# Kernel tuning notes

Measured on AMD Instinct MI355X. Metric: run time of the kernel, lower is better.

## Reference

```python
import jax, jax.numpy as jnp
import numpy as np

N_NODE = 50000
N_EDGE = 640000
IN_DIM = 128
OUT_DIM = 128
ATTN_DIM = 128
N_REL = 500
REL_VOCAB = 2 * N_REL + 3  # 1003


def setup_inputs() -> dict:
    key = jax.random.key(0)
    ks = jax.random.split(key, 10)
    hidden = jax.random.normal(ks[0], (N_NODE, IN_DIM), dtype=jnp.float32)
    sub = jax.random.randint(ks[1], (N_EDGE,), 0, N_NODE)
    rel = jax.random.randint(ks[2], (N_EDGE,), 0, REL_VOCAB)
    obj = jax.random.randint(ks[3], (N_EDGE,), 0, N_NODE)
    zero = jnp.zeros((N_EDGE,), dtype=jnp.int64 if jax.config.read('jax_enable_x64') else jnp.int32)
    # edges layout: [:,2]=rel, [:,4]=sub, [:,5]=obj (other columns unused)
    edges = jnp.stack([zero, zero, rel, zero, sub, obj], axis=1)
    old_nodes_new_idx = jax.random.randint(ks[4], (N_NODE,), 0, N_NODE)
    s = 1.0 / np.sqrt(IN_DIM)
    rela_embed = jax.random.normal(ks[5], (REL_VOCAB, IN_DIM), dtype=jnp.float32)
    Ws_attn = jax.random.uniform(ks[6], (IN_DIM, ATTN_DIM), minval=-s, maxval=s, dtype=jnp.float32)
    Wr_attn = jax.random.uniform(ks[7], (IN_DIM, ATTN_DIM), minval=-s, maxval=s, dtype=jnp.float32)
    sa = 1.0 / np.sqrt(ATTN_DIM)
    w_alpha_w = jax.random.uniform(ks[8], (ATTN_DIM, 1), minval=-sa, maxval=sa, dtype=jnp.float32)
    w_alpha_b = jnp.zeros((1,), dtype=jnp.float32)
    W_h = jax.random.uniform(ks[9], (IN_DIM, OUT_DIM), minval=-s, maxval=s, dtype=jnp.float32)
    return {
        'hidden': hidden, 'edges': edges, 'n_node': N_NODE,
        'old_nodes_new_idx': old_nodes_new_idx,
        'rela_embed': rela_embed, 'Ws_attn': Ws_attn, 'Wr_attn': Wr_attn,
        'w_alpha_w': w_alpha_w, 'w_alpha_b': w_alpha_b, 'W_h': W_h,
    }


def reference(hidden, edges, n_node, old_nodes_new_idx,
              rela_embed, Ws_attn, Wr_attn, w_alpha_w, w_alpha_b, W_h):
    sub = edges[:, 4]
    rel = edges[:, 2]
    obj = edges[:, 5]
    hs = hidden[sub]                 # [E, in_dim] gather
    hr = rela_embed[rel]             # [E, in_dim] gather
    message = hs + hr                # [E, in_dim]
    attn_h = jax.nn.relu(hs @ Ws_attn + hr @ Wr_attn)          # [E, attn_dim]
    alpha = jax.nn.sigmoid(attn_h @ w_alpha_w + w_alpha_b)     # [E, 1]
    message = alpha * message
    message_agg = jax.ops.segment_sum(message, obj, num_segments=n_node)  # [N, in_dim]
    hidden_new = message_agg @ W_h   # act is identity by default
    return hidden_new
```

## Files before the change

### kernel.cpp

```cpp
#include <hip/hip_runtime.h>

typedef float f4 __attribute__((ext_vector_type(4)));
typedef float f2 __attribute__((ext_vector_type(2)));
typedef float f32x4 __attribute__((ext_vector_type(4)));
typedef short bf16x8 __attribute__((ext_vector_type(8)));
typedef unsigned short u16x8 __attribute__((ext_vector_type(8)));

__device__ inline unsigned short f2bf(float f) {
  unsigned u = __float_as_uint(f);
  return (unsigned short)((u + 0x7FFF + ((u >> 16) & 1)) >> 16);
}

__global__ __launch_bounds__(256) void prep(
    const float* __restrict__ Ws, const float* __restrict__ Wr,
    const float* __restrict__ Wh, const int* __restrict__ edges, int n_edge,
    unsigned short* __restrict__ WsT, unsigned short* __restrict__ WrT,
    unsigned short* __restrict__ WhT, int* __restrict__ counts,
    uint2* __restrict__ epk) {
  const int t = threadIdx.x;
  int b = blockIdx.x;
  if (b < 192) {
    int wsel = b >> 6;
    const float* W = wsel == 0 ? Ws : (wsel == 1 ? Wr : Wh);
    unsigned short* WT = wsel == 0 ? WsT : (wsel == 1 ? WrT : WhT);
    int e = (b & 63) * 256 + t;
    int cc = e >> 7, kk = e & 127;
    WT[e] = f2bf(W[kk * 128 + cc]);
    return;
  }
  b -= 192;
  int e = b * 256 + t;
  if (e < n_edge) {
    int rel = edges[(size_t)e * 6 + 2];
    int2 so = *(const int2*)(edges + (size_t)e * 6 + 4);
    atomicAdd(&counts[so.y], 1);
    epk[e] = make_uint2((unsigned)so.x | ((unsigned)rel << 17), (unsigned)so.y);
  }
}

__global__ __launch_bounds__(256) void gemm_dual(
    const float* __restrict__ hidden, int M, int nbN,
    const float* __restrict__ rela, int relv,
    const unsigned short* __restrict__ WsT, const unsigned short* __restrict__ WrT,
    const unsigned short* __restrict__ WhT,
    char* __restrict__ rec, char* __restrict__ relrec) {
  __shared__ __align__(16) char lds[81920];
  const int t = threadIdx.x;
  int b = blockIdx.x;
  const float* src;
  const unsigned short* WxT;
  char* out;
  int rows, row0;
  if (b < nbN) { src = hidden; WxT = WsT; out = rec; rows = M; row0 = b * 64; }
  else { src = rela; WxT = WrT; out = relrec; rows = relv; row0 = (b - nbN) * 64; }

#pragma unroll
  for (int i = 0; i < 8; ++i) {
    int m = i * 256 + t;
    int sw = (m * 16) ^ (((m >> 4) & 7) << 4);
    *(u16x8*)(lds + 16384 + sw) = ((const u16x8*)WxT)[m];
    *(u16x8*)(lds + 49152 + sw) = ((const u16x8*)WhT)[m];
  }
#pragma unroll
  for (int i = 0; i < 4; ++i) {
    int m = i * 256 + t;
    int r = m >> 4, c = m & 15;
    int gr = row0 + r;
    if (gr > rows - 1) gr = rows - 1;
    const float* s = src + (size_t)gr * 128 + c * 8;
    f4 lo = *(const f4*)s, hi = *(const f4*)(s + 4);
    u16x8 v;
    v[0] = f2bf(lo.x); v[1] = f2bf(lo.y); v[2] = f2bf(lo.z); v[3] = f2bf(lo.w);
    v[4] = f2bf(hi.x); v[5] = f2bf(hi.y); v[6] = f2bf(hi.z); v[7] = f2bf(hi.w);
    *(u16x8*)(lds + ((m * 16) ^ ((r & 7) << 4))) = v;
  }
  __syncthreads();

  const int w = t >> 6, l = t & 63, lr = l & 15, lg = l >> 4;
  const int rowA = w * 16 + lr;
  bf16x8 afr[4];
#pragma unroll
  for (int k0 = 0; k0 < 4; ++k0)
    afr[k0] = *(const bf16x8*)(lds + rowA * 256 + ((k0 * 64 + lg * 16) ^ ((rowA & 7) << 4)));

  {
    f32x4 acc[8] = {};
#pragma unroll
    for (int k0 = 0; k0 < 4; ++k0) {
      int kb = k0 * 64 + lg * 16;
#pragma unroll
      for (int c0 = 0; c0 < 8; ++c0) {
        int cr = c0 * 16 + lr;
        bf16x8 bfr = *(const bf16x8*)(lds + 16384 + cr * 256 + (kb ^ ((cr & 7) << 4)));
        acc[c0] = __builtin_amdgcn_mfma_f32_16x16x32_bf16(afr[k0], bfr, acc[c0], 0, 0, 0);
      }
    }
#pragma unroll
    for (int c0 = 0; c0 < 8; ++c0) {
      int col = c0 * 16 + lr;
#pragma unroll
      for (int j = 0; j < 4; ++j) {
        int grow = row0 + w * 16 + lg * 4 + j;
        if (grow < rows) {
          unsigned pk = __builtin_amdgcn_cvt_pk_fp8_f32(acc[c0][j], acc[c0][j], 0, false);
          *(unsigned char*)(out + (size_t)grow * 384 + 256 + col) = (unsigned char)pk;
        }
      }
    }
  }
  {
    f32x4 acc[8] = {};
#pragma unroll
    for (int k0 = 0; k0 < 4; ++k0) {
      int kb = k0 * 64 + lg * 16;
#pragma unroll
      for (int c0 = 0; c0 < 8; ++c0) {
        int cr = c0 * 16 + lr;
        bf16x8 bfr = *(const bf16x8*)(lds + 49152 + cr * 256 + (kb ^ ((cr & 7) << 4)));
        acc[c0] = __builtin_amdgcn_mfma_f32_16x16x32_bf16(afr[k0], bfr, acc[c0], 0, 0, 0);
      }
    }
#pragma unroll
    for (int c0 = 0; c0 < 8; ++c0) {
      int col = c0 * 16 + lr;
#pragma unroll
      for (int j = 0; j < 4; ++j) {
        int grow = row0 + w * 16 + lg * 4 + j;
        if (grow < rows)
          *(unsigned short*)(out + (size_t)grow * 384 + col * 2) = f2bf(acc[c0][j]);
      }
    }
  }
}

__global__ __launch_bounds__(256) void scan_lookback(
    const int* __restrict__ counts, int M, int n_edge, int* __restrict__ status,
    int* __restrict__ offsets, int* __restrict__ cursor) {
  const int t = threadIdx.x, b = blockIdx.x;
  const int idx = b * 256 + t;
  int c = (idx < M) ? counts[idx] : 0;
  const int lane = t & 63, w = t >> 6;
  int s = c;
  for (int off = 1; off < 64; off <<= 1) {
    int o = __shfl_up(s, off, 64);
    if (lane >= off) s += o;
  }
  __shared__ int wsum[4], wpre[4];
  __shared__ int blk_prefix;
  if (lane == 63) wsum[w] = s;
  __syncthreads();
  if (t == 0) {
    int r = 0;
#pragma unroll
    for (int i = 0; i < 4; ++i) { wpre[i] = r; r += wsum[i]; }
    unsigned pub = ((b == 0 ? 2u : 1u) << 30) | (unsigned)r;
    __hip_atomic_store(&status[b], (int)pub, __ATOMIC_RELEASE, __HIP_MEMORY_SCOPE_AGENT);
    if (b == 0) blk_prefix = 0;
  }
  __syncthreads();
  if (b > 0 && w == 0) {
    int prefix = 0;
    int k = b - 1;
    for (;;) {
      int j = k - lane;
      unsigned v;
      if (j >= 0) {
        do {
          v = (unsigned)__hip_atomic_load(&status[j], __ATOMIC_ACQUIRE,
                                          __HIP_MEMORY_SCOPE_AGENT);
        } while ((v >> 30) == 0u);
      } else {
        v = 2u << 30;
      }
      int val = (int)(v & 0x3FFFFFFFu);
      unsigned long long incl = __ballot((v >> 30) == 2u);
      int l = (int)__ffsll(incl) - 1;
      int contrib = (l >= 0) ? ((lane <= l) ? val : 0) : val;
#pragma unroll
      for (int off = 32; off; off >>= 1) contrib += __shfl_xor(contrib, off, 64);
      prefix += contrib;
      if (l >= 0) break;
      k -= 64;
    }
    if (lane == 0) {
      blk_prefix = prefix;
      int total = wpre[3] + wsum[3];
      __hip_atomic_store(&status[b], (int)((2u << 30) | (unsigned)(prefix + total)),
                         __ATOMIC_RELEASE, __HIP_MEMORY_SCOPE_AGENT);
    }
  }
  __syncthreads();
  int excl = blk_prefix + wpre[w] + s - c;
  if (idx < M) { offsets[idx] = excl; cursor[idx] = excl; }
  if (idx == 0) offsets[M] = n_edge;
}

__global__ __launch_bounds__(256) void scatter_kernel(const uint2* __restrict__ epk,
                                                      int n_edge, int* __restrict__ cursor,
                                                      unsigned* __restrict__ esr) {
  int e = blockIdx.x * 256 + threadIdx.x;
  if (e < n_edge) {
    uint2 pe = epk[e];
    int pos = atomicAdd(&cursor[pe.y], 1);
    esr[pos] = pe.x;
  }
}

template <bool HI>
__device__ inline f2 pk8(unsigned u) {
  return __builtin_amdgcn_cvt_pk_f32_fp8(u, HI);
}

__device__ inline float edge_alpha(uint2 as, uint2 ar, const f2* wap, float bb) {
  f2 s0 = pk8<false>(as.x) + pk8<false>(ar.x);
  f2 s1 = pk8<true>(as.x) + pk8<true>(ar.x);
  f2 s2 = pk8<false>(as.y) + pk8<false>(ar.y);
  f2 s3 = pk8<true>(as.y) + pk8<true>(ar.y);
  s0.x = fmaxf(s0.x, 0.f); s0.y = fmaxf(s0.y, 0.f);
  s1.x = fmaxf(s1.x, 0.f); s1.y = fmaxf(s1.y, 0.f);
  s2.x = fmaxf(s2.x, 0.f); s2.y = fmaxf(s2.y, 0.f);
  s3.x = fmaxf(s3.x, 0.f); s3.y = fmaxf(s3.y, 0.f);
  f2 pp = s0 * wap[0];
  pp += s1 * wap[1];
  pp += s2 * wap[2];
  pp += s3 * wap[3];
  float p = pp.x + pp.y;
#pragma unroll
  for (int off = 1; off <= 8; off <<= 1) p += __shfl_xor(p, off, 64);
  return __builtin_amdgcn_rcpf(1.f + __builtin_amdgcn_exp2f(-(p + bb)));
}

__global__ __launch_bounds__(256) void node_agg(
    const int* __restrict__ offsets, const unsigned* __restrict__ esr,
    const char* __restrict__ rec, const char* __restrict__ relrec,
    float* __restrict__ out,
    const float* __restrict__ w_alpha, const float* __restrict__ w_b, int M) {
  const int lane = threadIdx.x & 63;
  const int g = lane >> 4, gl = lane & 15;
  const int n = (int)((blockIdx.x * 256u + threadIdx.x) >> 6);
  if (n >= M) return;
  const unsigned bH = gl * 16u, bA = 256u + gl * 8u;
  const float LOG2E = 1.44269504f;
  f2 wap[4];
#pragma unroll
  for (int k = 0; k < 4; ++k) wap[k] = ((const f2*)w_alpha)[gl * 4 + k] * LOG2E;
  const float bb = w_b[0] * LOG2E;

  const int beg = offsets[n], end = offsets[n + 1];
  f2 acc2[4] = {};

  for (int i = beg + g; i < end; i += 8) {
    const bool has2 = (i + 4) < end;
    unsigned u1 = esr[i];
    unsigned u2 = has2 ? esr[i + 4] : u1;
    unsigned o1x = (u1 & 0x1FFFFu) * 384u, o1y = (u1 >> 17) * 384u;
    unsigned o2x = (u2 & 0x1FFFFu) * 384u, o2y = (u2 >> 17) * 384u;

    u16x8 h1 = *(const u16x8*)(rec + o1x + bH);
    uint2 as1 = *(const uint2*)(rec + o1x + bA);
    u16x8 r1 = *(const u16x8*)(relrec + o1y + bH);
    uint2 ar1 = *(const uint2*)(relrec + o1y + bA);
    u16x8 h2 = *(const u16x8*)(rec + o2x + bH);
    uint2 as2 = *(const uint2*)(rec + o2x + bA);
    u16x8 r2 = *(const u16x8*)(relrec + o2y + bH);
    uint2 ar2 = *(const uint2*)(relrec + o2y + bA);

    float al1 = edge_alpha(as1, ar1, wap, bb);
    float al2 = edge_alpha(as2, ar2, wap, bb);
    if (!has2) al2 = 0.f;

    const uint4 hu1 = *(const uint4*)&h1, ru1 = *(const uint4*)&r1;
    const uint4 hu2 = *(const uint4*)&h2, ru2 = *(const uint4*)&r2;
    const unsigned hd1[4] = {hu1.x, hu1.y, hu1.z, hu1.w};
    const unsigned rd1[4] = {ru1.x, ru1.y, ru1.z, ru1.w};
    const unsigned hd2[4] = {hu2.x, hu2.y, hu2.z, hu2.w};
    const unsigned rd2[4] = {ru2.x, ru2.y, ru2.z, ru2.w};
#pragma unroll
    for (int k = 0; k < 4; ++k) {
      f2 m1, m2;
      m1.x = __uint_as_float(hd1[k] << 16) + __uint_as_float(rd1[k] << 16);
      m1.y = __uint_as_float(hd1[k] & 0xFFFF0000u) + __uint_as_float(rd1[k] & 0xFFFF0000u);
      m2.x = __uint_as_float(hd2[k] << 16) + __uint_as_float(rd2[k] << 16);
      m2.y = __uint_as_float(hd2[k] & 0xFFFF0000u) + __uint_as_float(rd2[k] & 0xFFFF0000u);
      acc2[k] += al1 * m1;
      acc2[k] += al2 * m2;
    }
  }

#pragma unroll
  for (int k = 0; k < 4; ++k) {
    acc2[k].x += __shfl_xor(acc2[k].x, 16, 64);
    acc2[k].y += __shfl_xor(acc2[k].y, 16, 64);
    acc2[k].x += __shfl_xor(acc2[k].x, 32, 64);
    acc2[k].y += __shfl_xor(acc2[k].y, 32, 64);
  }
  if (g == 0) {
    f4 lo = {acc2[0].x, acc2[0].y, acc2[1].x, acc2[1].y};
    f4 hi = {acc2[2].x, acc2[2].y, acc2[3].x, acc2[3].y};
    float* dst = out + (size_t)n * 128 + gl * 8;
    *(f4*)dst = lo;
    *(f4*)(dst + 4) = hi;
  }
}

extern "C" void kernel_launch(void* const* d_in, const int* in_sizes, int n_in,
                              void* d_out, int out_size, void* d_ws, size_t ws_size,
                              hipStream_t stream) {
  const float* hidden = (const float*)d_in[0];
  const int* edges = (const int*)d_in[1];
  const float* rela = (const float*)d_in[4];
  const float* Ws = (const float*)d_in[5];
  const float* Wr = (const float*)d_in[6];
  const float* wa = (const float*)d_in[7];
  const float* wb = (const float*)d_in[8];
  const float* Wh = (const float*)d_in[9];

  const int M = in_sizes[0] / 128;
  const int n_edge = in_sizes[1] / 6;
  const int relv = in_sizes[4] / 128;
  const int NB = (M + 255) / 256;
  const int BE = (n_edge + 255) / 256;

  char* ws = (char*)d_ws;
  size_t off = 0;
  char* rec = ws; off += ((size_t)M * 384 + 255) & ~255ull;
  char* relrec = ws + off; off += ((size_t)relv * 384 + 255) & ~255ull;
  unsigned short* WsT = (unsigned short*)(ws + off); off += 32768;
  unsigned short* WrT = (unsigned short*)(ws + off); off += 32768;
  unsigned short* WhT = (unsigned short*)(ws + off); off += 32768;
  unsigned* esr = (unsigned*)(ws + off); off += ((size_t)n_edge * 4 + 255) & ~255ull;
  uint2* epk = (uint2*)(ws + off); off += (size_t)n_edge * 8;
  int* counts = (int*)(ws + off); off += (size_t)M * 4;
  int* status = (int*)(ws + off); off += 4096;
  int* offsets = (int*)(ws + off); off += ((size_t)(M + 1) * 4 + 255) & ~255ull;
  int* cursor = (int*)(ws + off);
  float* out = (float*)d_out;

  (void)hipMemsetAsync(counts, 0, (size_t)M * 4 + 4096, stream);

  prep<<<192 + BE, 256, 0, stream>>>(Ws, Wr, Wh, edges, n_edge, WsT, WrT, WhT,
                                     counts, epk);

  const int nbN = (M + 63) / 64;
  gemm_dual<<<nbN + (relv + 63) / 64, 256, 0, stream>>>(hidden, M, nbN, rela, relv,
                                                        WsT, WrT, WhT, rec, relrec);

  scan_lookback<<<NB, 256, 0, stream>>>(counts, M, n_edge, status, offsets, cursor);
  scatter_kernel<<<BE, 256, 0, stream>>>(epk, n_edge, cursor, esr);

  node_agg<<<(M * 64 + 255) / 256, 256, 0, stream>>>(offsets, esr, rec, relrec,
                                                     out, wa, wb, M);
}
```

Measured before the change: 150.3 us.

## Record edge rank at count time and stage GEMM outputs through LDS for coalesced stores

The counting pass keeps the atomicAdd return value as a per-destination rank and packs it into the edge record. Placement then becomes a plain offset+rank write, which removes the second pass of atomics on a cursor array and the cursor writes in the scan. Separately, the dual GEMM epilogue writes its fp8 and bf16 results into LDS and then stores whole rows with 16-byte vector writes instead of scattered byte and short stores. The cost is extra barriers and LDS traffic, plus an implicit limit that node ids fit in 17 bits and ranks in 15 bits.

New measurement: 122.7 us, median of 3. 18.4% less time.

```diff
diff --git a/kernel.cpp b/kernel.cpp
--- a/kernel.cpp
+++ b/kernel.cpp
@@ -33,8 +33,9 @@
   if (e < n_edge) {
     int rel = edges[(size_t)e * 6 + 2];
     int2 so = *(const int2*)(edges + (size_t)e * 6 + 4);
-    atomicAdd(&counts[so.y], 1);
-    epk[e] = make_uint2((unsigned)so.x | ((unsigned)rel << 17), (unsigned)so.y);
+    unsigned rank = (unsigned)atomicAdd(&counts[so.y], 1);
+    epk[e] = make_uint2((unsigned)so.x | ((unsigned)rel << 17),
+                        (unsigned)so.y | (rank << 17));
   }
 }
 
@@ -95,19 +96,30 @@
         acc[c0] = __builtin_amdgcn_mfma_f32_16x16x32_bf16(afr[k0], bfr, acc[c0], 0, 0, 0);
       }
     }
+    __syncthreads();
 #pragma unroll
     for (int c0 = 0; c0 < 8; ++c0) {
       int col = c0 * 16 + lr;
 #pragma unroll
       for (int j = 0; j < 4; ++j) {
-        int grow = row0 + w * 16 + lg * 4 + j;
-        if (grow < rows) {
-          unsigned pk = __builtin_amdgcn_cvt_pk_fp8_f32(acc[c0][j], acc[c0][j], 0, false);
-          *(unsigned char*)(out + (size_t)grow * 384 + 256 + col) = (unsigned char)pk;
-        }
-      }
-    }
-  }
+        int row = w * 16 + lg * 4 + j;
+        unsigned pk = __builtin_amdgcn_cvt_pk_fp8_f32(acc[c0][j], acc[c0][j], 0, false);
+        *(unsigned char*)(lds + 16384 + row * 128 + col) = (unsigned char)pk;
+      }
+    }
+    __syncthreads();
+#pragma unroll
+    for (int it = 0; it < 2; ++it) {
+      int idx = it * 256 + t;
+      int row = idx >> 3, seg = idx & 7;
+      int grow = row0 + row;
+      if (grow < rows) {
+        uint4 v = *(const uint4*)(lds + 16384 + row * 128 + seg * 16);
+        *(uint4*)(out + (size_t)grow * 384 + 256 + seg * 16) = v;
+      }
+    }
+  }
+  __syncthreads();
   {
     f32x4 acc[8] = {};
 #pragma unroll
@@ -120,14 +132,25 @@
         acc[c0] = __builtin_amdgcn_mfma_f32_16x16x32_bf16(afr[k0], bfr, acc[c0], 0, 0, 0);
       }
     }
+    __syncthreads();
 #pragma unroll
     for (int c0 = 0; c0 < 8; ++c0) {
       int col = c0 * 16 + lr;
 #pragma unroll
       for (int j = 0; j < 4; ++j) {
-        int grow = row0 + w * 16 + lg * 4 + j;
-        if (grow < rows)
-          *(unsigned short*)(out + (size_t)grow * 384 + col * 2) = f2bf(acc[c0][j]);
+        int row = w * 16 + lg * 4 + j;
+        *(unsigned short*)(lds + 16384 + row * 256 + col * 2) = f2bf(acc[c0][j]);
+      }
+    }
+    __syncthreads();
+#pragma unroll
+    for (int it = 0; it < 4; ++it) {
+      int idx = it * 256 + t;
+      int row = idx >> 4, seg = idx & 15;
+      int grow = row0 + row;
+      if (grow < rows) {
+        uint4 v = *(const uint4*)(lds + 16384 + row * 256 + seg * 16);
+        *(uint4*)(out + (size_t)grow * 384 + seg * 16) = v;
       }
     }
   }
@@ -135,7 +158,7 @@
 
 __global__ __launch_bounds__(256) void scan_lookback(
     const int* __restrict__ counts, int M, int n_edge, int* __restrict__ status,
-    int* __restrict__ offsets, int* __restrict__ cursor) {
+    int* __restrict__ offsets) {
   const int t = threadIdx.x, b = blockIdx.x;
   const int idx = b * 256 + t;
   int c = (idx < M) ? counts[idx] : 0;
@@ -191,18 +214,19 @@
   }
   __syncthreads();
   int excl = blk_prefix + wpre[w] + s - c;
-  if (idx < M) { offsets[idx] = excl; cursor[idx] = excl; }
+  if (idx < M) offsets[idx] = excl;
   if (idx == 0) offsets[M] = n_edge;
 }
 
-__global__ __launch_bounds__(256) void scatter_kernel(const uint2* __restrict__ epk,
-                                                      int n_edge, int* __restrict__ cursor,
-                                                      unsigned* __restrict__ esr) {
+__global__ __launch_bounds__(256) void placement_kernel(const uint2* __restrict__ epk,
+                                                        int n_edge,
+                                                        const int* __restrict__ offsets,
+                                                        unsigned* __restrict__ esr) {
   int e = blockIdx.x * 256 + threadIdx.x;
   if (e < n_edge) {
     uint2 pe = epk[e];
-    int pos = atomicAdd(&cursor[pe.y], 1);
-    esr[pos] = pe.x;
+    unsigned obj = pe.y & 0x1FFFFu, rank = pe.y >> 17;
+    esr[offsets[obj] + rank] = pe.x;
   }
 }
 
@@ -333,7 +357,6 @@
   int* counts = (int*)(ws + off); off += (size_t)M * 4;
   int* status = (int*)(ws + off); off += 4096;
   int* offsets = (int*)(ws + off); off += ((size_t)(M + 1) * 4 + 255) & ~255ull;
-  int* cursor = (int*)(ws + off);
   float* out = (float*)d_out;
 
   (void)hipMemsetAsync(counts, 0, (size_t)M * 4 + 4096, stream);
@@ -345,8 +368,8 @@
   gemm_dual<<<nbN + (relv + 63) / 64, 256, 0, stream>>>(hidden, M, nbN, rela, relv,
                                                         WsT, WrT, WhT, rec, relrec);
 
-  scan_lookback<<<NB, 256, 0, stream>>>(counts, M, n_edge, status, offsets, cursor);
-  scatter_kernel<<<BE, 256, 0, stream>>>(epk, n_edge, cursor, esr);
+  scan_lookback<<<NB, 256, 0, stream>>>(counts, M, n_edge, status, offsets);
+  placement_kernel<<<BE, 256, 0, stream>>>(epk, n_edge, offsets, esr);
 
   node_agg<<<(M * 64 + 255) / 256, 256, 0, stream>>>(offsets, esr, rec, relrec,
                                                      out, wa, wb, M);
```
